# Kernel tuning notes

Hardware: AMD Instinct MI355X
Metric: run time of the kernel (lower is better)

Reference implementation:

```python
import jax, jax.numpy as jnp
import numpy as np

N = 100000   # num nodes
E = 600000   # num edges
H = 128      # hidden dim
R = 8        # num relations
B = 4        # num bases


def setup_inputs() -> dict:
    key = jax.random.key(0)
    ks = jax.random.split(key, 12)
    return {
        "node_ids": jnp.arange(N, dtype=jnp.int64 if jax.config.jax_enable_x64 else jnp.int32),
        "src": jax.random.randint(ks[0], (E,), 0, N),
        "dst": jax.random.randint(ks[1], (E,), 0, N),
        "etype": jax.random.randint(ks[2], (E,), 0, R),
        "embedding": jax.random.normal(ks[3], (N, H), dtype=jnp.float32),
        "V1": jax.random.normal(ks[4], (B, H, H), dtype=jnp.float32) * 0.05,
        "comp1": jax.random.normal(ks[5], (R, B), dtype=jnp.float32),
        "loop1": jax.random.normal(ks[6], (H, H), dtype=jnp.float32) * 0.05,
        "bias1": jax.random.normal(ks[7], (H,), dtype=jnp.float32) * 0.05,
        "V2": jax.random.normal(ks[8], (B, H, H), dtype=jnp.float32) * 0.05,
        "comp2": jax.random.normal(ks[9], (R, B), dtype=jnp.float32),
        "loop2": jax.random.normal(ks[10], (H, H), dtype=jnp.float32) * 0.05,
        "bias2": jax.random.normal(ks[11], (H,), dtype=jnp.float32) * 0.05,
    }


def _rgcn_layer(h, src, dst, etype, V, comp, loopW, bias, activate):
    # basis decomposition: W_r = sum_b comp[r,b] * V[b]   -> [R, in, out]
    W = jnp.einsum('rb,bio->rio', comp, V)
    # transform all nodes under all relations once (avoids per-edge GEMM): [N, R, out]
    hw = jnp.einsum('ni,rio->nro', h, W)
    # gather per-edge message for its (src, relation): [E, out]
    m = hw[src, etype]
    # scatter-sum aggregation at destination nodes
    agg = jax.ops.segment_sum(m, dst, num_segments=h.shape[0])
    out = agg + bias + h @ loopW  # bias + self-loop
    return jax.nn.relu(out) if activate else out


def reference(node_ids, src, dst, etype, embedding,
              V1, comp1, loop1, bias1,
              V2, comp2, loop2, bias2):
    h = embedding[node_ids]                       # EmbeddingLayer
    h = _rgcn_layer(h, src, dst, etype, V1, comp1, loop1, bias1, activate=True)
    h = _rgcn_layer(h, src, dst, etype, V2, comp2, loop2, bias2, activate=False)
    return h
```

## Files before the change

### kernel.cpp

```cpp
#include <hip/hip_runtime.h>
#include <hip/hip_bf16.h>

#define NN 100000
#define NE 600000
#define HH 128
#define NB 4
#define TILE 2048
#define NTILES ((NN + TILE - 1) / TILE)

typedef __attribute__((ext_vector_type(8))) short bf16x8;
typedef __attribute__((ext_vector_type(4))) float f32x4;
typedef __attribute__((ext_vector_type(4))) float vfloat4;
typedef __attribute__((ext_vector_type(4))) unsigned short ushort4v;

static __device__ __forceinline__ short f2bf(float f) {
  unsigned u = __float_as_uint(f);
  unsigned r = (u + 0x7fffu + ((u >> 16) & 1u)) >> 16;
  return (short)r;
}

static __device__ __forceinline__ float bf2f(short s) {
  unsigned u = (unsigned)(unsigned short)s;
  return __uint_as_float(u << 16);
}

__global__ __launch_bounds__(256) void build_wt(const float* __restrict__ V,
                                                const float* __restrict__ loopW,
                                                short* __restrict__ W8)
{
  int idx = blockIdx.x * blockDim.x + threadIdx.x;
  int j  = idx & 7;
  int o  = (idx >> 3) & 127;
  int kb = idx >> 10;
  int k  = kb * 8 + j;
  float v;
  if (k < 512) v = V[(size_t)k * HH + o];
  else         v = loopW[(size_t)(k - 512) * HH + o];
  W8[idx] = f2bf(v);
}

__global__ __launch_bounds__(256) void cast_h(const float* __restrict__ in,
                                              short* __restrict__ out)
{
  const int n8 = NN * HH / 8;
  for (int i = blockIdx.x * blockDim.x + threadIdx.x; i < n8; i += gridDim.x * blockDim.x) {
    const vfloat4* p = reinterpret_cast<const vfloat4*>(in + i * 8);
    vfloat4 a = p[0], b = p[1];
    bf16x8 o;
#pragma unroll
    for (int j = 0; j < 4; ++j) { o[j] = f2bf(a[j]); o[j + 4] = f2bf(b[j]); }
    reinterpret_cast<bf16x8*>(out)[i] = o;
  }
}


__global__ __launch_bounds__(256) void hist_deg(const int* __restrict__ dst,
                                                int* __restrict__ deg)
{
  int e = blockIdx.x * blockDim.x + threadIdx.x;
  if (e < NE) atomicAdd(&deg[dst[e]], 1);
}

__global__ __launch_bounds__(256) void scan_tiles(const int* __restrict__ deg,
                                                  int* __restrict__ tilesum)
{
  __shared__ int red[256];
  const int tid = threadIdx.x;
  int base = blockIdx.x * TILE + tid * 8;
  int s = 0;
#pragma unroll
  for (int j = 0; j < 8; ++j) {
    int i = base + j;
    if (i < NN) s += deg[i];
  }
  red[tid] = s;
  __syncthreads();
  for (int off = 128; off > 0; off >>= 1) {
    if (tid < off) red[tid] += red[tid + off];
    __syncthreads();
  }
  if (tid == 0) tilesum[blockIdx.x] = red[0];
}

__global__ __launch_bounds__(256) void scan_final(const int* deg,
                                                  const int* __restrict__ tilesum,
                                                  int* __restrict__ rowptr,
                                                  int* cursor)
{
  __shared__ int lds[256];
  const int tid = threadIdx.x;
  int pre = 0;
  for (int t = 0; t < NTILES; ++t)
    if (t < blockIdx.x) pre += tilesum[t];

  int base = blockIdx.x * TILE + tid * 8;
  int d[8];
  int s = 0;
#pragma unroll
  for (int j = 0; j < 8; ++j) {
    int i = base + j;
    d[j] = (i < NN) ? deg[i] : 0;
    s += d[j];
  }
  lds[tid] = s;
  __syncthreads();
  for (int off = 1; off < 256; off <<= 1) {
    int t = (tid >= off) ? lds[tid - off] : 0;
    __syncthreads();
    lds[tid] += t;
    __syncthreads();
  }
  int run = pre + lds[tid] - s;
#pragma unroll
  for (int j = 0; j < 8; ++j) {
    int i = base + j;
    if (i < NN) {
      rowptr[i] = run;
      cursor[i] = run;
      run += d[j];
    }
  }
  if (blockIdx.x == NTILES - 1 && tid == 255)
    rowptr[NN] = pre + lds[255];
}

__global__ __launch_bounds__(256) void scatter_edges(
    const int* __restrict__ src, const int* __restrict__ dst, const int* __restrict__ ety,
    int* __restrict__ cursor, int* __restrict__ csr)
{
  int e = blockIdx.x * blockDim.x + threadIdx.x;
  if (e >= NE) return;
  int d = dst[e];
  int p = atomicAdd(&cursor[d], 1);
  csr[p] = src[e] | (ety[e] << 20);
}

template<int FINAL>
__global__ __launch_bounds__(512, 6) void rgcn_fused(
    const int* __restrict__ rowptr, const int* __restrict__ csr,
    const float* __restrict__ comp,
    const short* __restrict__ hbf,
    const short* __restrict__ W8,
    const float* __restrict__ bias,
    short* __restrict__ outH,
    float* __restrict__ outF)
{
  __shared__ bf16x8 gl[32][64];
  __shared__ bf16x8 wl[2][512];

  const int tid  = threadIdx.x;
  const int wave = tid >> 6;
  const int lane = tid & 63;
  const int b  = lane >> 4;
  const int q  = lane & 15;
  const int base = blockIdx.x * 32;

  const int mt = wave >> 2;
  const int ct0 = (wave & 3) * 2;
  const int mynode = base + mt * 16 + q;

#pragma unroll 1
  for (int pp = 0; pp < 2; ++pp) {
    const int row0 = wave * 4 + pp * 2;
    const int row1 = row0 + 1;
    int       i0 = __builtin_amdgcn_readfirstlane(rowptr[base + row0]);
    const int E0 = __builtin_amdgcn_readfirstlane(rowptr[base + row0 + 1]);
    int       i1 = E0;
    const int E1 = __builtin_amdgcn_readfirstlane(rowptr[base + row1 + 1]);

    float a0[8] = {0.f, 0.f, 0.f, 0.f, 0.f, 0.f, 0.f, 0.f};
    float a1[8] = {0.f, 0.f, 0.f, 0.f, 0.f, 0.f, 0.f, 0.f};

    while (i0 < E0 || i1 < E1) {
      const bool d0 = i0 < E0, d1 = i1 < E1;
      bf16x8 H[8];
      float  C[8];
      if (d0) {
#pragma unroll
        for (int j = 0; j < 4; ++j) {
          const int idx = i0 + j;
          const bool v = idx < E0;
          const int e = csr[v ? idx : E0 - 1];
          H[j] = reinterpret_cast<const bf16x8*>(hbf + (size_t)(e & 0xFFFFF) * HH)[q];
          C[j] = v ? comp[(e >> 20) * NB + b] : 0.f;
        }
      }
      if (d1) {
#pragma unroll
        for (int j = 0; j < 4; ++j) {
          const int idx = i1 + j;
          const bool v = idx < E1;
          const int e = csr[v ? idx : E1 - 1];
          H[4 + j] = reinterpret_cast<const bf16x8*>(hbf + (size_t)(e & 0xFFFFF) * HH)[q];
          C[4 + j] = v ? comp[(e >> 20) * NB + b] : 0.f;
        }
      }
      if (d0) {
#pragma unroll
        for (int j = 0; j < 4; ++j)
#pragma unroll
          for (int k = 0; k < 8; ++k) a0[k] += bf2f(H[j][k]) * C[j];
        i0 += 4;
      }
      if (d1) {
#pragma unroll
        for (int j = 0; j < 4; ++j)
#pragma unroll
          for (int k = 0; k < 8; ++k) a1[k] += bf2f(H[4 + j][k]) * C[4 + j];
        i1 += 4;
      }
    }

    bf16x8 o0, o1;
#pragma unroll
    for (int j = 0; j < 8; ++j) { o0[j] = f2bf(a0[j]); o1[j] = f2bf(a1[j]); }
    gl[row0][lane ^ (row0 & 7)] = o0;
    gl[row1][lane ^ (row1 & 7)] = o1;
  }

  const bf16x8* ha = reinterpret_cast<const bf16x8*>(hbf + (size_t)mynode * HH);
  bf16x8 hreg[4];
#pragma unroll
  for (int j = 0; j < 4; ++j) hreg[j] = ha[j * 4 + b];

  const bf16x8* wsrc = reinterpret_cast<const bf16x8*>(W8);
  wl[0][tid] = wsrc[tid];
  __syncthreads();

  const int r  = q;
  const int g8 = b;

  f32x4 acc0 = {0.f, 0.f, 0.f, 0.f};
  f32x4 acc1 = {0.f, 0.f, 0.f, 0.f};

#pragma unroll 1
  for (int ks = 0; ks < 20; ++ks) {
    const int cur = ks & 1;
    bf16x8 nxt;
    if (ks < 19) nxt = wsrc[(ks + 1) * 512 + tid];
    bf16x8 a = (ks < 16) ? gl[mt * 16 + r][(ks * 4 + g8) ^ (r & 7)] : hreg[ks - 16];
    bf16x8 w0 = wl[cur][g8 * 128 + (ct0 + 0) * 16 + r];
    bf16x8 w1 = wl[cur][g8 * 128 + (ct0 + 1) * 16 + r];
    acc0 = __builtin_amdgcn_mfma_f32_16x16x32_bf16(w0, a, acc0, 0, 0, 0);
    acc1 = __builtin_amdgcn_mfma_f32_16x16x32_bf16(w1, a, acc1, 0, 0, 0);
    if (ks < 19) wl[cur ^ 1][tid] = nxt;
    __syncthreads();
  }

#pragma unroll
  for (int c = 0; c < 2; ++c) {
    const f32x4 acc = c ? acc1 : acc0;
    const int o = (ct0 + c) * 16 + g8 * 4;
    vfloat4 bs = *reinterpret_cast<const vfloat4*>(bias + o);
    if (FINAL) {
      vfloat4 x;
#pragma unroll
      for (int rr = 0; rr < 4; ++rr) x[rr] = acc[rr] + bs[rr];
      reinterpret_cast<vfloat4*>(outF + (size_t)mynode * HH)[(ct0 + c) * 4 + g8] = x;
    } else {
      ushort4v s;
#pragma unroll
      for (int rr = 0; rr < 4; ++rr)
        s[rr] = (unsigned short)f2bf(fmaxf(acc[rr] + bs[rr], 0.f));
      reinterpret_cast<ushort4v*>(outH + (size_t)mynode * HH)[(ct0 + c) * 4 + g8] = s;
    }
  }
}

extern "C" void kernel_launch(void* const* d_in, const int* in_sizes, int n_in,
                              void* d_out, int out_size, void* d_ws, size_t ws_size,
                              hipStream_t stream)
{
  const int*   srcp  = (const int*)d_in[1];
  const int*   dstp  = (const int*)d_in[2];
  const int*   etp   = (const int*)d_in[3];
  const float* emb   = (const float*)d_in[4];
  const float* V1    = (const float*)d_in[5];
  const float* comp1 = (const float*)d_in[6];
  const float* loop1 = (const float*)d_in[7];
  const float* bias1 = (const float*)d_in[8];
  const float* V2    = (const float*)d_in[9];
  const float* comp2 = (const float*)d_in[10];
  const float* loop2 = (const float*)d_in[11];
  const float* bias2 = (const float*)d_in[12];
  float* out = (float*)d_out;

  char* ws = (char*)d_ws;
  short* Wt1     = (short*)(ws);
  short* Wt2     = (short*)(ws + 163840);
  short* hbf1    = (short*)(ws + 327680);
  short* hbf2    = (short*)(ws + 25927680);
  int*   deg     = (int*)  (ws + 51527680);
  int*   rowptr  = (int*)  (ws + 51927680);
  int*   csr     = (int*)  (ws + 52327696);
  int*   tilesum = (int*)  (ws + 54727696);

  const int fused_blocks = NN / 32;
  const int e_blocks     = (NE + 255) / 256;

  hipMemsetAsync(deg, 0, NN * sizeof(int), stream);
  hipLaunchKernelGGL(hist_deg, dim3(e_blocks), dim3(256), 0, stream, dstp, deg);
  hipLaunchKernelGGL(scan_tiles, dim3(NTILES), dim3(256), 0, stream, deg, tilesum);
  hipLaunchKernelGGL(scan_final, dim3(NTILES), dim3(256), 0, stream,
                     deg, tilesum, rowptr, deg);
  hipLaunchKernelGGL(scatter_edges, dim3(e_blocks), dim3(256), 0, stream,
                     srcp, dstp, etp, deg, csr);

  hipLaunchKernelGGL(build_wt, dim3(320), dim3(256), 0, stream, V1, loop1, Wt1);
  hipLaunchKernelGGL(build_wt, dim3(320), dim3(256), 0, stream, V2, loop2, Wt2);
  hipLaunchKernelGGL(cast_h, dim3(2048), dim3(256), 0, stream, emb, hbf1);

  hipLaunchKernelGGL((rgcn_fused<0>), dim3(fused_blocks), dim3(512), 0, stream,
                     rowptr, csr, comp1, hbf1, Wt1, bias1, hbf2, (float*)nullptr);

  hipLaunchKernelGGL((rgcn_fused<1>), dim3(fused_blocks), dim3(512), 0, stream,
                     rowptr, csr, comp2, hbf2, Wt2, bias2, (short*)nullptr, out);
}
```

Measured before the change: 321.1 us.

## Stage epilogue through LDS for coalesced row stores and prefetch first weight slice

The epilogue now writes MFMA accumulator fragments into a swizzled shared-memory tile, then reads them back so each thread stores contiguous 16-byte chunks of whole output rows. This replaces the scattered per-lane stores with coalesced global writes. The first weight-slice load is also issued before the gather phase so its latency overlaps the aggregation. The cost is an extra barrier and an LDS round trip, plus one more register held live across the gather loop.

```diff
diff --git a/kernel.cpp b/kernel.cpp
--- a/kernel.cpp
+++ b/kernel.cpp
@@ -159,6 +159,9 @@
   const int ct0 = (wave & 3) * 2;
   const int mynode = base + mt * 16 + q;
 
+  const bf16x8* wsrc = reinterpret_cast<const bf16x8*>(W8);
+  bf16x8 w0reg = wsrc[tid];
+
 #pragma unroll 1
   for (int pp = 0; pp < 2; ++pp) {
     const int row0 = wave * 4 + pp * 2;
@@ -223,8 +226,7 @@
 #pragma unroll
   for (int j = 0; j < 4; ++j) hreg[j] = ha[j * 4 + b];
 
-  const bf16x8* wsrc = reinterpret_cast<const bf16x8*>(W8);
-  wl[0][tid] = wsrc[tid];
+  wl[0][tid] = w0reg;
   __syncthreads();
 
   const int r  = q;
@@ -247,22 +249,52 @@
     __syncthreads();
   }
 
-#pragma unroll
-  for (int c = 0; c < 2; ++c) {
-    const f32x4 acc = c ? acc1 : acc0;
-    const int o = (ct0 + c) * 16 + g8 * 4;
-    vfloat4 bs = *reinterpret_cast<const vfloat4*>(bias + o);
-    if (FINAL) {
+  if (FINAL) {
+    float* glf = reinterpret_cast<float*>(gl);
+#pragma unroll
+    for (int c = 0; c < 2; ++c) {
+      const f32x4 acc = c ? acc1 : acc0;
+      const int row = mt * 16 + r;
+      const int o = (ct0 + c) * 16 + g8 * 4;
+      vfloat4 bs = *reinterpret_cast<const vfloat4*>(bias + o);
       vfloat4 x;
 #pragma unroll
       for (int rr = 0; rr < 4; ++rr) x[rr] = acc[rr] + bs[rr];
-      reinterpret_cast<vfloat4*>(outF + (size_t)mynode * HH)[(ct0 + c) * 4 + g8] = x;
-    } else {
-      ushort4v s;
+      const int s = (ct0 + c) * 4 + g8;
+      const int phys = s ^ (row & 7);
+      *reinterpret_cast<vfloat4*>(glf + row * 128 + phys * 4) = x;
+    }
+    __syncthreads();
+#pragma unroll
+    for (int p = 0; p < 2; ++p) {
+      const int flat = p * 512 + tid;
+      const int row = flat >> 5, s = flat & 31;
+      const int phys = s ^ (row & 7);
+      vfloat4 x = *reinterpret_cast<const vfloat4*>(glf + row * 128 + phys * 4);
+      *reinterpret_cast<vfloat4*>(outF + (size_t)(base + row) * HH + s * 4) = x;
+    }
+  } else {
+    short* glb = reinterpret_cast<short*>(gl);
+#pragma unroll
+    for (int c = 0; c < 2; ++c) {
+      const f32x4 acc = c ? acc1 : acc0;
+      const int row = mt * 16 + r;
+      const int o = (ct0 + c) * 16 + g8 * 4;
+      vfloat4 bs = *reinterpret_cast<const vfloat4*>(bias + o);
+      ushort4v sv;
 #pragma unroll
       for (int rr = 0; rr < 4; ++rr)
-        s[rr] = (unsigned short)f2bf(fmaxf(acc[rr] + bs[rr], 0.f));
-      reinterpret_cast<ushort4v*>(outH + (size_t)mynode * HH)[(ct0 + c) * 4 + g8] = s;
+        sv[rr] = (unsigned short)f2bf(fmaxf(acc[rr] + bs[rr], 0.f));
+      const int u8 = (ct0 + c) * 4 + g8;
+      const int phys16 = (u8 >> 1) ^ (row & 7);
+      *reinterpret_cast<ushort4v*>(glb + row * 128 + phys16 * 8 + (u8 & 1) * 4) = sv;
+    }
+    __syncthreads();
+    {
+      const int row = tid >> 4, s16 = tid & 15;
+      const int phys = s16 ^ (row & 7);
+      bf16x8 x = *reinterpret_cast<const bf16x8*>(glb + row * 128 + phys * 8);
+      *reinterpret_cast<bf16x8*>(outH + (size_t)(base + row) * HH + s16 * 8) = x;
     }
   }
 }
```

Measured after the change: 317.9 us. No clear change (-1.0%).
